# Performance work log

Measured on AMD Instinct MI355X. Metric: run time of the kernel, lower is better.

The kernel has to match this reference:

```python
import jax, jax.numpy as jnp
import numpy as np

B, T, H, W, C = 1, 16, 56, 56, 256
NH = 8
WS = (8, 7, 7)
SS = (4, 3, 3)
HID = 4 * C
N = WS[0] * WS[1] * WS[2]  # 392 tokens per window


def _rel_index(ws):
    wt, wh, ww = ws
    coords = np.stack(np.meshgrid(np.arange(wt), np.arange(wh), np.arange(ww), indexing='ij'))
    cf = coords.reshape(3, -1)
    rel = (cf[:, :, None] - cf[:, None, :]).transpose(1, 2, 0)
    rel[..., 0] += wt - 1
    rel[..., 1] += wh - 1
    rel[..., 2] += ww - 1
    rel[..., 0] *= (2 * wh - 1) * (2 * ww - 1)
    rel[..., 1] *= 2 * ww - 1
    return rel.sum(-1)  # (N, N) int


def _win_part_np(x, ws):
    b, t, h, w, c = x.shape
    x = x.reshape(b, t // ws[0], ws[0], h // ws[1], ws[1], w // ws[2], ws[2], c)
    return x.transpose(0, 1, 3, 5, 2, 4, 6, 7).reshape(-1, ws[0] * ws[1] * ws[2], c)


def _attn_mask(t, h, w, ws, ss):
    # static numpy construction of the shifted-window mask (nW, N, N)
    img = np.zeros((1, t, h, w, 1), dtype=np.float32)
    cnt = 0
    for d in (slice(-ws[0]), slice(-ws[0], -ss[0]), slice(-ss[0], None)):
        for hh in (slice(-ws[1]), slice(-ws[1], -ss[1]), slice(-ss[1], None)):
            for ww_ in (slice(-ws[2]), slice(-ws[2], -ss[2]), slice(-ss[2], None)):
                img[:, d, hh, ww_, :] = cnt
                cnt += 1
    mw = _win_part_np(img, ws).squeeze(-1)  # (nW, N)
    diff = mw[:, None, :] - mw[:, :, None]
    return np.where(diff != 0, np.float32(-100.0), np.float32(0.0))


_RPI = jnp.asarray(_rel_index(WS).reshape(-1))
_MASK = jnp.asarray(_attn_mask(T, H, W, WS, SS))  # (nW, N, N)


def _ln(x, g, b, eps=1e-5):
    mu = x.mean(-1, keepdims=True)
    var = ((x - mu) ** 2).mean(-1, keepdims=True)
    return (x - mu) * jax.lax.rsqrt(var + eps) * g + b


def _win_part(x, ws):
    b, t, h, w, c = x.shape
    x = x.reshape(b, t // ws[0], ws[0], h // ws[1], ws[1], w // ws[2], ws[2], c)
    return x.transpose(0, 1, 3, 5, 2, 4, 6, 7).reshape(-1, ws[0] * ws[1] * ws[2], c)


def _win_rev(win, ws, t, h, w):
    b = win.shape[0] // (t * h * w // (ws[0] * ws[1] * ws[2]))
    x = win.reshape(b, t // ws[0], h // ws[1], w // ws[2], ws[0], ws[1], ws[2], -1)
    return x.transpose(0, 1, 4, 2, 5, 3, 6, 7).reshape(b, t, h, w, -1)


def setup_inputs() -> dict:
    key = jax.random.key(0)
    ks = jax.random.split(key, 16)
    n_bias = (2 * WS[0] - 1) * (2 * WS[1] - 1) * (2 * WS[2] - 1)
    return {
        'x': jax.random.normal(ks[0], (B, T, H, W, C), jnp.float32),
        'norm1_g': jnp.ones((C,), jnp.float32),
        'norm1_b': jnp.zeros((C,), jnp.float32),
        'qkv_w': 0.02 * jax.random.normal(ks[1], (3 * C, C), jnp.float32),
        'qkv_b': jnp.zeros((3 * C,), jnp.float32),
        'rpb_table': 0.02 * jax.random.normal(ks[2], (n_bias, NH), jnp.float32),
        'proj_w': 0.02 * jax.random.normal(ks[3], (C, C), jnp.float32),
        'proj_b': jnp.zeros((C,), jnp.float32),
        'norm2_g': jnp.ones((C,), jnp.float32),
        'norm2_b': jnp.zeros((C,), jnp.float32),
        'fc1_w': 0.02 * jax.random.normal(ks[4], (HID, C), jnp.float32),
        'fc1_b': jnp.zeros((HID,), jnp.float32),
        'fc2_w': 0.02 * jax.random.normal(ks[5], (C, HID), jnp.float32),
        'fc2_b': jnp.zeros((C,), jnp.float32),
    }


def reference(x, norm1_g, norm1_b, qkv_w, qkv_b, rpb_table, proj_w, proj_b,
              norm2_g, norm2_b, fc1_w, fc1_b, fc2_w, fc2_b):
    hd = C // NH
    scale = hd ** -0.5
    shortcut = x
    h1 = _ln(x, norm1_g, norm1_b)
    # cyclic shift
    h1 = jnp.roll(h1, (-SS[0], -SS[1], -SS[2]), axis=(1, 2, 3))
    xw = _win_part(h1, WS)  # (B_, N, C)
    B_ = xw.shape[0]
    qkv = xw @ qkv_w.T + qkv_b  # (B_, N, 3C)
    qkv = qkv.reshape(B_, N, 3, NH, hd).transpose(2, 0, 3, 1, 4)
    q, k, v = qkv[0], qkv[1], qkv[2]  # (B_, NH, N, hd)
    attn = jnp.einsum('bhnd,bhmd->bhnm', q * scale, k)
    bias = rpb_table[_RPI].reshape(N, N, NH).transpose(2, 0, 1)  # (NH, N, N)
    attn = attn + bias[None]
    nW = _MASK.shape[0]
    attn = attn.reshape(B_ // nW, nW, NH, N, N) + _MASK[None, :, None]
    attn = jax.nn.softmax(attn, axis=-1).reshape(B_, NH, N, N)
    out = jnp.einsum('bhnm,bhmd->bhnd', attn, v).transpose(0, 2, 1, 3).reshape(B_, N, C)
    out = out @ proj_w.T + proj_b
    out = _win_rev(out, WS, T, H, W)
    out = jnp.roll(out, (SS[0], SS[1], SS[2]), axis=(1, 2, 3))
    x = shortcut + out
    # MLP with residual
    h2 = _ln(x, norm2_g, norm2_b)
    h2 = jax.nn.gelu(h2 @ fc1_w.T + fc1_b, approximate=False)
    return x + (h2 @ fc2_w.T + fc2_b)
```

## Files before the change

### kernel.cpp

```cpp
#include <hip/hip_runtime.h>
#include <hip/hip_bf16.h>
#include <cmath>

typedef unsigned short u16;
typedef unsigned int u32;

using bf16x8 = __attribute__((ext_vector_type(8))) short;
using f32x4  = __attribute__((ext_vector_type(4))) float;

__device__ __forceinline__ float b2f(u16 u) {
  union { u32 i; float f; } x; x.i = ((u32)u) << 16; return x.f;
}
__device__ __forceinline__ u16 f2b(float f) {
  union { float f; u32 i; } x; x.f = f;
  u32 r = x.i + 0x7fffu + ((x.i >> 16) & 1u);
  return (u16)(r >> 16);
}
__device__ __forceinline__ u32 cvtpk(float lo, float hi) {
  u32 r;
  asm("v_cvt_pk_bf16_f32 %0, %1, %2" : "=v"(r) : "v"(lo), "v"(hi));
  return r;
}
__device__ __forceinline__ float vexp2(float x) {
  float r;
  asm("v_exp_f32 %0, %1" : "=v"(r) : "v"(x));
  return r;
}
__device__ __forceinline__ void gload_lds16(const u16* g, u16* l) {
  __builtin_amdgcn_global_load_lds(
      (const __attribute__((address_space(1))) unsigned int*)g,
      (__attribute__((address_space(3))) unsigned int*)l, 16, 0, 0);
}

__global__ __launch_bounds__(256) void castw(const float* __restrict__ qkvw,
                                             const float* __restrict__ projw,
                                             const float* __restrict__ fc1w,
                                             const float* __restrict__ fc2w,
                                             u16* __restrict__ o) {
  int i = blockIdx.x * 256 + threadIdx.x;
  const float* src;
  int off;
  if (i < 196608)      { src = qkvw;  off = 0; }
  else if (i < 262144) { src = projw; off = 196608; }
  else if (i < 524288) { src = fc1w;  off = 262144; }
  else                 { src = fc2w;  off = 524288; }
  o[i] = f2b(src[i - off]);
}

__global__ __launch_bounds__(256) void bias_k(const float* __restrict__ rpb,
                                              u16* __restrict__ biasB,
                                              float* __restrict__ rowmax) {
  const int b = blockIdx.x;
  const int sl = b / 25, qt = b - sl * 25;
  const int head = sl & 7, cls = sl >> 3;
  const int tb = (cls >> 2) & 1, hb = (cls >> 1) & 1, wb = cls & 1;
  const int tid = threadIdx.x;
  const int lm = tid >> 4, kl = tid & 15;
  int q = qt * 16 + lm; if (q > 391) q = 391;
  const int ti = q / 49, rem = q - ti * 49, hi = rem / 7, wi = rem - hi * 7;
  const int cq = ti * 169 + hi * 13 + wi;
  const int rtq = tb ? (ti < 4 ? 1 : 2) : 0;
  const int rhq = hb ? (hi < 4 ? 1 : 2) : 0;
  const int rwq = wb ? (wi < 4 ? 1 : 2) : 0;
  const int labq = rtq * 9 + rhq * 3 + rwq;
  float mx = -3e38f;
  u16* ob = biasB + (size_t)b * 6400 + tid;
  for (int t = 0; t < 25; t++) {
    int k = t * 16 + kl;
    float v;
    if (k < 392) {
      int tk = k / 49, rk = k - tk * 49, hk = rk / 7, wk = rk - hk * 7;
      int ck = tk * 169 + hk * 13 + wk;
      float bv = rpb[(cq - ck + 1267) * 8 + head];
      int rt = tb ? (tk < 4 ? 1 : 2) : 0;
      int rh = hb ? (hk < 4 ? 1 : 2) : 0;
      int rw = wb ? (wk < 4 ? 1 : 2) : 0;
      if (rt * 9 + rh * 3 + rw != labq) bv -= 100.f;
      v = bv * 1.4426950408889634f;
      mx = fmaxf(mx, v);
    } else {
      v = -2081.f;
    }
    ob[t * 256] = f2b(v);
  }
  mx = fmaxf(mx, __shfl_xor(mx, 1, 64));
  mx = fmaxf(mx, __shfl_xor(mx, 2, 64));
  mx = fmaxf(mx, __shfl_xor(mx, 4, 64));
  mx = fmaxf(mx, __shfl_xor(mx, 8, 64));
  if (kl == 0) rowmax[sl * 392 + q] = mx;
}

__global__ __launch_bounds__(256) void ln_k(const float* __restrict__ src,
                                            const float* __restrict__ g,
                                            const float* __restrict__ b,
                                            u16* __restrict__ dst, int shifted) {
  const int wid = threadIdx.x >> 6, lane = threadIdx.x & 63;
  const int row = blockIdx.x * 4 + wid;
  int srow;
  if (shifted) {
    int widx = row / 392, n = row - widx * 392;
    int wt = widx >> 6, wh = (widx >> 3) & 7, ww = widx & 7;
    int ti = n / 49, rem = n - ti * 49, hi = rem / 7, wi = rem - hi * 7;
    int t = (wt * 8 + ti + 4) & 15;
    int h = wh * 7 + hi + 3; if (h >= 56) h -= 56;
    int w = ww * 7 + wi + 3; if (w >= 56) w -= 56;
    srow = (t * 56 + h) * 56 + w;
  } else {
    srow = row;
  }
  float4 v = *(const float4*)(src + (size_t)srow * 256 + lane * 4);
  float s = v.x + v.y + v.z + v.w;
  float sq = v.x * v.x + v.y * v.y + v.z * v.z + v.w * v.w;
  for (int o = 1; o < 64; o <<= 1) {
    s += __shfl_xor(s, o, 64);
    sq += __shfl_xor(sq, o, 64);
  }
  float mu = s * (1.0f / 256.0f);
  float rstd = rsqrtf(sq * (1.0f / 256.0f) - mu * mu + 1e-5f);
  float4 gg = *(const float4*)(g + lane * 4);
  float4 bb = *(const float4*)(b + lane * 4);
  ushort4 ov;
  ov.x = f2b((v.x - mu) * rstd * gg.x + bb.x);
  ov.y = f2b((v.y - mu) * rstd * gg.y + bb.y);
  ov.z = f2b((v.z - mu) * rstd * gg.z + bb.z);
  ov.w = f2b((v.w - mu) * rstd * gg.w + bb.w);
  *(ushort4*)(dst + (size_t)row * 256 + lane * 4) = ov;
}

template <int EPI>
__global__ __launch_bounds__(512) void gemm_k(const u16* __restrict__ A,
                                              const u16* __restrict__ Bw,
                                              int K, int tilesN,
                                              const float* __restrict__ bias,
                                              u16* __restrict__ outb,
                                              float* __restrict__ outf,
                                              const float* __restrict__ res,
                                              float qscale) {
  __shared__ __align__(16) u16 As[2][256 * 32];
  __shared__ __align__(16) u16 Bs[2][128 * 32];
  const int tid = threadIdx.x;
  const int swzb = ((int)blockIdx.x & 7) * ((int)gridDim.x >> 3) +
                   ((int)blockIdx.x >> 3);
  const int tm = swzb / tilesN, tn = swzb - tm * tilesN;
  const int wid = tid >> 6, lane = tid & 63;
  const int wm = wid >> 1, wn = wid & 1;
  const int lm = lane & 15, lk = lane >> 4;
  f32x4 acc[4][4] = {};
  const u16* Ap = A + (size_t)tm * 256 * K;
  const u16* Bp = Bw + (size_t)tn * 128 * K;

  const int sA0 = wid * 128;
  const int sB0 = wid * 64;
  const int nt = K >> 5;

#define STAGE(bufi, kk)                                                       \
  {                                                                           \
    int S = sA0 + lane, r = S >> 2, cs = S & 3;                               \
    gload_lds16(Ap + (size_t)r * K + (kk) + ((cs ^ ((r >> 1) & 3)) << 3),     \
                &As[bufi][sA0 * 8]);                                          \
    S = sA0 + 64 + lane; r = S >> 2; cs = S & 3;                              \
    gload_lds16(Ap + (size_t)r * K + (kk) + ((cs ^ ((r >> 1) & 3)) << 3),     \
                &As[bufi][(sA0 + 64) * 8]);                                   \
    S = sB0 + lane; r = S >> 2; cs = S & 3;                                   \
    gload_lds16(Bp + (size_t)r * K + (kk) + ((cs ^ ((r >> 1) & 3)) << 3),     \
                &Bs[bufi][sB0 * 8]);                                          \
  }

  STAGE(0, 0);
  __syncthreads();
  for (int t = 0; t < nt; t++) {
    const int cur = t & 1;
    if (t + 1 < nt) STAGE(cur ^ 1, (t + 1) << 5);
    bf16x8 af[4], bfr[4];
#pragma unroll
    for (int f = 0; f < 4; f++) {
      int ra = wm * 64 + f * 16 + lm;
      int rb = wn * 64 + f * 16 + lm;
      af[f] = *(const bf16x8*)((const char*)&As[cur][0] + ra * 64 +
                               ((lk ^ ((ra >> 1) & 3)) << 4));
      bfr[f] = *(const bf16x8*)((const char*)&Bs[cur][0] + rb * 64 +
                                ((lk ^ ((rb >> 1) & 3)) << 4));
    }
#pragma unroll
    for (int fm = 0; fm < 4; fm++)
#pragma unroll
      for (int fn = 0; fn < 4; fn++)
        acc[fm][fn] = __builtin_amdgcn_mfma_f32_16x16x32_bf16(
            af[fm], bfr[fn], acc[fm][fn], 0, 0, 0);
    __syncthreads();
  }
#undef STAGE

  const int rbase = tm * 256 + wm * 64, cbase = tn * 128 + wn * 64;
#pragma unroll
  for (int fm = 0; fm < 4; fm++) {
#pragma unroll
    for (int fn = 0; fn < 4; fn++) {
      const int col = cbase + fn * 16 + lm;
#pragma unroll
      for (int r = 0; r < 4; r++) {
        const int row = rbase + fm * 16 + lk * 4 + r;
        float v = acc[fm][fn][r] + bias[col];
        if (EPI == 0) {
          int s = col >> 8, rem = col & 255, head = rem >> 5, d = rem & 31;
          int widx = row / 392, n = row - widx * 392;
          size_t o;
          if (s == 2) {
            o = 25690112u + (((size_t)(widx * 8 + head)) * 32 + d) * 400 + n;
          } else {
            if (s == 0) v *= qscale;
            o = (size_t)s * 12845056u +
                (((size_t)(widx * 8 + head)) * 392 + n) * 32 + d;
          }
          outb[o] = f2b(v);
        } else if (EPI == 1) {
          int widx = row / 392, n = row - widx * 392;
          int wt = widx >> 6, wh = (widx >> 3) & 7, ww = widx & 7;
          int ti = n / 49, rem2 = n - ti * 49, hi = rem2 / 7, wi = rem2 - hi * 7;
          int t = (wt * 8 + ti + 4) & 15;
          int h = wh * 7 + hi + 3; if (h >= 56) h -= 56;
          int w = ww * 7 + wi + 3; if (w >= 56) w -= 56;
          size_t dr = ((size_t)(t * 56 + h)) * 56 + w;
          outf[dr * 256 + col] = res[dr * 256 + col] + v;
        } else if (EPI == 2) {
          float gv = 0.5f * v * (1.0f + erff(v * 0.70710678f));
          outb[(size_t)row * 1024 + col] = f2b(gv);
        } else {
          outf[(size_t)row * 256 + col] = res[(size_t)row * 256 + col] + v;
        }
      }
    }
  }
}

__global__ __launch_bounds__(256) void attn_k(const u16* __restrict__ qg,
                                              const u16* __restrict__ kg,
                                              const u16* __restrict__ vTg,
                                              const u16* __restrict__ biasB,
                                              const float* __restrict__ rowmax,
                                              u16* __restrict__ attno) {
  __shared__ __align__(16) char lds[60928];
  const int bid = blockIdx.x;
  const int widx = bid >> 3;
  const int tid = threadIdx.x;
  const size_t base = (size_t)bid * 12544;
  const int tb = (widx >> 6) & 1;
  const int hb = (((widx >> 3) & 7) == 7) ? 1 : 0;
  const int wb = ((widx & 7) == 7) ? 1 : 0;
  const int sl = (tb * 4 + hb * 2 + wb) * 8 + (bid & 7);
  const int VOFF = 25600;

#pragma unroll
  for (int i = 0; i < 6; i++) {
    int s = i * 256 + tid, r = s >> 2, cs = s & 3;
    gload_lds16(kg + base + r * 32 + ((cs ^ ((r >> 1) & 3)) << 3),
                (u16*)(lds + (size_t)(i * 256 + (tid & ~63)) * 16));
  }
  if (tid < 32) {
    int s = 1536 + tid, r = s >> 2, cs = s & 3;
    gload_lds16(kg + base + r * 32 + ((cs ^ ((r >> 1) & 3)) << 3),
                (u16*)(lds + (size_t)1536 * 16));
  }
  if (tid < 128) ((u32*)(lds + 25088))[tid] = 0u;
  {
    const u16* vsrc = vTg + (size_t)bid * 12800;
    for (int idx = tid; idx < 3200; idx += 256) {
      int d = idx / 100, c4 = idx - d * 100;
      *(ushort4*)(lds + VOFF + d * 848 + c4 * 8) =
          *(const ushort4*)(vsrc + d * 400 + c4 * 4);
    }
    for (int idx = tid; idx < 512; idx += 256) {
      int d = idx >> 4, e = idx & 15;
      *(u16*)(lds + VOFF + d * 848 + 800 + e * 2) = 0;
    }
  }
  __syncthreads();

  const int w = tid >> 6, lane = tid & 63;
  const int g = lane >> 4, lm = lane & 15;
  char* PqW = lds + 52736 + w * 2048 + lm * 128;
  const int swz = (lm & 7) << 4;
  const int kswz = ((lm >> 1) & 3);

  for (int qt = w; qt < 25; qt += 4) {
    const int q = qt * 16 + lm;
    const int qr = q < 391 ? q : 391;
    bf16x8 qf = *(const bf16x8*)(qg + base + (size_t)qr * 32 + g * 8);
    const u16* bp = biasB + ((size_t)(sl * 25 + qt) * 25) * 256 + lm * 16 + 4 * g;
    const float rmb = rowmax[sl * 392 + qr];
    f32x4 st[25];
#pragma unroll
    for (int t = 0; t < 25; t++) {
      ushort4 bb = *(const ushort4*)(bp + t * 256);
      f32x4 bacc = {b2f(bb.x), b2f(bb.y), b2f(bb.z), b2f(bb.w)};
      bf16x8 kf = *(const bf16x8*)(lds + (16 * t + lm) * 64 + ((g ^ kswz) << 4));
      st[t] = __builtin_amdgcn_mfma_f32_16x16x32_bf16(kf, qf, bacc, 0, 0, 0);
    }
    float m = -3e38f;
#pragma unroll
    for (int t = 0; t < 25; t++)
      m = fmaxf(m, fmaxf(fmaxf(st[t][0], st[t][1]), fmaxf(st[t][2], st[t][3])));
    m = fmaxf(m, __shfl_xor(m, 16, 64));
    m = fmaxf(m, __shfl_xor(m, 32, 64));
    m += rmb;

    float sum = 0.f;
    f32x4 oa0 = {0.f, 0.f, 0.f, 0.f}, oa1 = {0.f, 0.f, 0.f, 0.f};
#pragma unroll
    for (int p = 0; p < 6; p++) {
#pragma unroll
      for (int tl = 0; tl < 4; tl++) {
        int t = 4 * p + tl;
        float e0 = vexp2(st[t][0] - m), e1 = vexp2(st[t][1] - m);
        float e2 = vexp2(st[t][2] - m), e3 = vexp2(st[t][3] - m);
        sum += (e0 + e1) + (e2 + e3);
        uint2 pp;
        pp.x = cvtpk(e0, e1);
        pp.y = cvtpk(e2, e3);
        *(uint2*)(PqW + ((32 * tl + 8 * g) ^ swz)) = pp;
      }
      asm volatile("s_waitcnt lgkmcnt(0)" ::: "memory");
      __builtin_amdgcn_sched_barrier(0);
#pragma unroll
      for (int cl = 0; cl < 2; cl++) {
        int c = 2 * p + cl;
        bf16x8 pf = *(const bf16x8*)(PqW + ((64 * cl + 16 * g) ^ swz));
        const char* vrow = lds + VOFF + 64 * c + 16 * g;
        bf16x8 v0 = *(const bf16x8*)(vrow + lm * 848);
        bf16x8 v1 = *(const bf16x8*)(vrow + (16 + lm) * 848);
        oa0 = __builtin_amdgcn_mfma_f32_16x16x32_bf16(pf, v0, oa0, 0, 0, 0);
        oa1 = __builtin_amdgcn_mfma_f32_16x16x32_bf16(pf, v1, oa1, 0, 0, 0);
      }
      __builtin_amdgcn_sched_barrier(0);
    }
    {
      float e0 = vexp2(st[24][0] - m), e1 = vexp2(st[24][1] - m);
      float e2 = vexp2(st[24][2] - m), e3 = vexp2(st[24][3] - m);
      sum += (e0 + e1) + (e2 + e3);
      uint2 pp;
      pp.x = cvtpk(e0, e1);
      pp.y = cvtpk(e2, e3);
      *(uint2*)(PqW + ((8 * g) ^ swz)) = pp;
      uint2 zz; zz.x = 0u; zz.y = 0u;
      *(uint2*)(PqW + ((32 + 8 * g) ^ swz)) = zz;
      asm volatile("s_waitcnt lgkmcnt(0)" ::: "memory");
      __builtin_amdgcn_sched_barrier(0);
      bf16x8 pf = *(const bf16x8*)(PqW + ((16 * g) ^ swz));
      const char* vrow = lds + VOFF + 64 * 12 + 16 * g;
      bf16x8 v0 = *(const bf16x8*)(vrow + lm * 848);
      bf16x8 v1 = *(const bf16x8*)(vrow + (16 + lm) * 848);
      oa0 = __builtin_amdgcn_mfma_f32_16x16x32_bf16(pf, v0, oa0, 0, 0, 0);
      oa1 = __builtin_amdgcn_mfma_f32_16x16x32_bf16(pf, v1, oa1, 0, 0, 0);
      __builtin_amdgcn_sched_barrier(0);
    }
    sum += __shfl_xor(sum, 16, 64);
    sum += __shfl_xor(sum, 32, 64);
    const float inv = 1.f / sum;
#pragma unroll
    for (int r = 0; r < 4; r++) {
      int qq = qt * 16 + 4 * g + r;
      if (qq < 392) {
        u16* op = attno + ((size_t)(widx * 392 + qq)) * 256 + (bid & 7) * 32;
        op[lm] = f2b(oa0[r] * inv);
        op[16 + lm] = f2b(oa1[r] * inv);
      }
    }
  }
}

extern "C" void kernel_launch(void* const* d_in, const int* in_sizes, int n_in,
                              void* d_out, int out_size, void* d_ws,
                              size_t ws_size, hipStream_t stream) {
  const float* x     = (const float*)d_in[0];
  const float* n1g   = (const float*)d_in[1];
  const float* n1b   = (const float*)d_in[2];
  const float* qkvw  = (const float*)d_in[3];
  const float* qkvb  = (const float*)d_in[4];
  const float* rpb   = (const float*)d_in[5];
  const float* projw = (const float*)d_in[6];
  const float* projb = (const float*)d_in[7];
  const float* n2g   = (const float*)d_in[8];
  const float* n2b   = (const float*)d_in[9];
  const float* fc1w  = (const float*)d_in[10];
  const float* fc1b  = (const float*)d_in[11];
  const float* fc2w  = (const float*)d_in[12];
  const float* fc2b  = (const float*)d_in[13];

  const size_t NEED = 130547712;
  if (ws_size < NEED) return;

  char* ws = (char*)d_ws;
  u16* xw      = (u16*)(ws + 0LL);
  u16* qb      = (u16*)(ws + 25690112LL);
  u16* attno   = (u16*)(ws + 0LL);
  u16* hid     = (u16*)(ws + 0LL);
  u16* biasB   = (u16*)(ws + 103284736LL);
  float* rmx   = (float*)(ws + 123764736LL);
  u16* h2      = (u16*)(ws + 103284736LL);
  u16* wq      = (u16*)(ws + 128974848LL);
  u16* wp      = (u16*)(ws + 129368064LL);
  u16* w1      = (u16*)(ws + 129499136LL);
  u16* w2      = (u16*)(ws + 130023424LL);
  float* xres  = (float*)d_out;

  castw<<<3072, 256, 0, stream>>>(qkvw, projw, fc1w, fc2w, wq);
  bias_k<<<1600, 256, 0, stream>>>(rpb, biasB, rmx);

  ln_k<<<12544, 256, 0, stream>>>(x, n1g, n1b, xw, 1);
  gemm_k<0><<<196 * 6, 512, 0, stream>>>(
      xw, wq, 256, 6, qkvb, qb, nullptr, nullptr,
      0.17677669529663687f * 1.4426950408889634f);
  attn_k<<<1024, 256, 0, stream>>>(qb, qb + 12845056, qb + 2 * 12845056, biasB,
                                   rmx, attno);
  gemm_k<1><<<196 * 2, 512, 0, stream>>>(attno, wp, 256, 2, projb, nullptr,
                                         xres, x, 0.f);
  ln_k<<<12544, 256, 0, stream>>>(xres, n2g, n2b, h2, 0);
  gemm_k<2><<<196 * 8, 512, 0, stream>>>(h2, w1, 256, 8, fc1b, hid, nullptr,
                                         nullptr, 0.f);
  gemm_k<3><<<196 * 2, 512, 0, stream>>>(hid, w2, 1024, 2, fc2b, nullptr,
                                         (float*)d_out, xres, 0.f);
}
```

Before: 330.1 us.

## Redistribute softmax probabilities via ds_bpermute instead of LDS staging

```diff
diff --git a/kernel.cpp b/kernel.cpp
--- a/kernel.cpp
+++ b/kernel.cpp
@@ -25,6 +25,9 @@
   float r;
   asm("v_exp_f32 %0, %1" : "=v"(r) : "v"(x));
   return r;
+}
+__device__ __forceinline__ u32 bperm(int byteaddr, u32 v) {
+  return __builtin_amdgcn_ds_bpermute(byteaddr, v);
 }
 __device__ __forceinline__ void gload_lds16(const u16* g, u16* l) {
   __builtin_amdgcn_global_load_lds(
@@ -233,13 +236,11 @@
   }
 }
 
-__global__ __launch_bounds__(256) void attn_k(const u16* __restrict__ qg,
-                                              const u16* __restrict__ kg,
-                                              const u16* __restrict__ vTg,
-                                              const u16* __restrict__ biasB,
-                                              const float* __restrict__ rowmax,
-                                              u16* __restrict__ attno) {
-  __shared__ __align__(16) char lds[60928];
+__global__ __launch_bounds__(256, 3) void attn_k(
+    const u16* __restrict__ qg, const u16* __restrict__ kg,
+    const u16* __restrict__ vTg, const u16* __restrict__ biasB,
+    const float* __restrict__ rowmax, u16* __restrict__ attno) {
+  __shared__ __align__(16) char lds[52736];
   const int bid = blockIdx.x;
   const int widx = bid >> 3;
   const int tid = threadIdx.x;
@@ -278,9 +279,9 @@
 
   const int w = tid >> 6, lane = tid & 63;
   const int g = lane >> 4, lm = lane & 15;
-  char* PqW = lds + 52736 + w * 2048 + lm * 128;
-  const int swz = (lm & 7) << 4;
   const int kswz = ((lm >> 1) & 3);
+  const int srcA = (((lane >> 4) & 1) << 7) + (lm << 2);
+  const bool hi = (g >= 2);
 
   for (int qt = w; qt < 25; qt += 4) {
     const int q = qt * 16 + lm;
@@ -307,51 +308,35 @@
     float sum = 0.f;
     f32x4 oa0 = {0.f, 0.f, 0.f, 0.f}, oa1 = {0.f, 0.f, 0.f, 0.f};
 #pragma unroll
-    for (int p = 0; p < 6; p++) {
-#pragma unroll
-      for (int tl = 0; tl < 4; tl++) {
-        int t = 4 * p + tl;
-        float e0 = vexp2(st[t][0] - m), e1 = vexp2(st[t][1] - m);
-        float e2 = vexp2(st[t][2] - m), e3 = vexp2(st[t][3] - m);
-        sum += (e0 + e1) + (e2 + e3);
-        uint2 pp;
-        pp.x = cvtpk(e0, e1);
-        pp.y = cvtpk(e2, e3);
-        *(uint2*)(PqW + ((32 * tl + 8 * g) ^ swz)) = pp;
+    for (int c = 0; c < 13; c++) {
+      float e00 = vexp2(st[2 * c][0] - m), e01 = vexp2(st[2 * c][1] - m);
+      float e02 = vexp2(st[2 * c][2] - m), e03 = vexp2(st[2 * c][3] - m);
+      sum += (e00 + e01) + (e02 + e03);
+      u32 a0 = cvtpk(e00, e01), a1 = cvtpk(e02, e03);
+      u32 b0, b1;
+      if (c < 12) {
+        float e10 = vexp2(st[2 * c + 1][0] - m), e11 = vexp2(st[2 * c + 1][1] - m);
+        float e12 = vexp2(st[2 * c + 1][2] - m), e13 = vexp2(st[2 * c + 1][3] - m);
+        sum += (e10 + e11) + (e12 + e13);
+        b0 = cvtpk(e10, e11);
+        b1 = cvtpk(e12, e13);
+      } else {
+        b0 = 0u; b1 = 0u;
       }
-      asm volatile("s_waitcnt lgkmcnt(0)" ::: "memory");
-      __builtin_amdgcn_sched_barrier(0);
-#pragma unroll
-      for (int cl = 0; cl < 2; cl++) {
-        int c = 2 * p + cl;
-        bf16x8 pf = *(const bf16x8*)(PqW + ((64 * cl + 16 * g) ^ swz));
-        const char* vrow = lds + VOFF + 64 * c + 16 * g;
-        bf16x8 v0 = *(const bf16x8*)(vrow + lm * 848);
-        bf16x8 v1 = *(const bf16x8*)(vrow + (16 + lm) * 848);
-        oa0 = __builtin_amdgcn_mfma_f32_16x16x32_bf16(pf, v0, oa0, 0, 0, 0);
-        oa1 = __builtin_amdgcn_mfma_f32_16x16x32_bf16(pf, v1, oa1, 0, 0, 0);
-      }
-      __builtin_amdgcn_sched_barrier(0);
-    }
-    {
-      float e0 = vexp2(st[24][0] - m), e1 = vexp2(st[24][1] - m);
-      float e2 = vexp2(st[24][2] - m), e3 = vexp2(st[24][3] - m);
-      sum += (e0 + e1) + (e2 + e3);
-      uint2 pp;
-      pp.x = cvtpk(e0, e1);
-      pp.y = cvtpk(e2, e3);
-      *(uint2*)(PqW + ((8 * g) ^ swz)) = pp;
-      uint2 zz; zz.x = 0u; zz.y = 0u;
-      *(uint2*)(PqW + ((32 + 8 * g) ^ swz)) = zz;
-      asm volatile("s_waitcnt lgkmcnt(0)" ::: "memory");
-      __builtin_amdgcn_sched_barrier(0);
-      bf16x8 pf = *(const bf16x8*)(PqW + ((16 * g) ^ swz));
-      const char* vrow = lds + VOFF + 64 * 12 + 16 * g;
+      u32 A0 = bperm(srcA, a0), B0 = bperm(srcA, b0);
+      u32 A1 = bperm(srcA, a1), B1 = bperm(srcA, b1);
+      u32 A2 = bperm(srcA + 64, a0), B2 = bperm(srcA + 64, b0);
+      u32 A3 = bperm(srcA + 64, a1), B3 = bperm(srcA + 64, b1);
+      union { u32 u[4]; bf16x8 v; } P;
+      P.u[0] = hi ? B0 : A0;
+      P.u[1] = hi ? B1 : A1;
+      P.u[2] = hi ? B2 : A2;
+      P.u[3] = hi ? B3 : A3;
+      const char* vrow = lds + VOFF + 64 * c + 16 * g;
       bf16x8 v0 = *(const bf16x8*)(vrow + lm * 848);
       bf16x8 v1 = *(const bf16x8*)(vrow + (16 + lm) * 848);
-      oa0 = __builtin_amdgcn_mfma_f32_16x16x32_bf16(pf, v0, oa0, 0, 0, 0);
-      oa1 = __builtin_amdgcn_mfma_f32_16x16x32_bf16(pf, v1, oa1, 0, 0, 0);
-      __builtin_amdgcn_sched_barrier(0);
+      oa0 = __builtin_amdgcn_mfma_f32_16x16x32_bf16(P.v, v0, oa0, 0, 0, 0);
+      oa1 = __builtin_amdgcn_mfma_f32_16x16x32_bf16(P.v, v1, oa1, 0, 0, 0);
     }
     sum += __shfl_xor(sum, 16, 64);
     sum += __shfl_xor(sum, 32, 64);
```

Result: slower. 471.5 us (+42.9%).

## Fuse LayerNorm2, FC1+GELU and FC2 into a single MLP kernel

Applied to the files above, without the earlier changes.

```diff
diff --git a/kernel.cpp b/kernel.cpp
--- a/kernel.cpp
+++ b/kernel.cpp
@@ -213,7 +213,7 @@
                 (((size_t)(widx * 8 + head)) * 392 + n) * 32 + d;
           }
           outb[o] = f2b(v);
-        } else if (EPI == 1) {
+        } else {
           int widx = row / 392, n = row - widx * 392;
           int wt = widx >> 6, wh = (widx >> 3) & 7, ww = widx & 7;
           int ti = n / 49, rem2 = n - ti * 49, hi = rem2 / 7, wi = rem2 - hi * 7;
@@ -222,12 +222,149 @@
           int w = ww * 7 + wi + 3; if (w >= 56) w -= 56;
           size_t dr = ((size_t)(t * 56 + h)) * 56 + w;
           outf[dr * 256 + col] = res[dr * 256 + col] + v;
-        } else if (EPI == 2) {
+        }
+      }
+    }
+  }
+}
+
+__global__ __launch_bounds__(256) void mlp_k(const float* __restrict__ xres,
+                                             const u16* __restrict__ w1,
+                                             const float* __restrict__ b1,
+                                             const u16* __restrict__ w2,
+                                             const float* __restrict__ b2,
+                                             const float* __restrict__ n2g,
+                                             const float* __restrict__ n2b,
+                                             float* __restrict__ out) {
+  __shared__ __align__(16) char lds[65536];
+  char* Abuf = lds;
+  char* Hs = lds + 32768;
+  u16* Ws = (u16*)(lds + 49152);
+
+  const int tid = threadIdx.x;
+  const int swzb = ((int)blockIdx.x & 7) * ((int)gridDim.x >> 3) +
+                   ((int)blockIdx.x >> 3);
+  const int row0 = swzb * 64;
+  const int w = tid >> 6, lane = tid & 63;
+  const int lm = lane & 15, g = lane >> 4;
+
+  {
+    float4 gg = *(const float4*)(n2g + lane * 4);
+    float4 bb = *(const float4*)(n2b + lane * 4);
+    for (int rr = 0; rr < 16; rr++) {
+      int r = w * 16 + rr;
+      float4 v = *(const float4*)(xres + (size_t)(row0 + r) * 256 + lane * 4);
+      float s = v.x + v.y + v.z + v.w;
+      float sq = v.x * v.x + v.y * v.y + v.z * v.z + v.w * v.w;
+      for (int o = 1; o < 64; o <<= 1) {
+        s += __shfl_xor(s, o, 64);
+        sq += __shfl_xor(sq, o, 64);
+      }
+      float mu = s * (1.0f / 256.0f);
+      float rstd = rsqrtf(sq * (1.0f / 256.0f) - mu * mu + 1e-5f);
+      uint2 pp;
+      pp.x = cvtpk((v.x - mu) * rstd * gg.x + bb.x,
+                   (v.y - mu) * rstd * gg.y + bb.y);
+      pp.y = cvtpk((v.z - mu) * rstd * gg.z + bb.z,
+                   (v.w - mu) * rstd * gg.w + bb.w);
+      *(uint2*)(Abuf + r * 512 + (((lane >> 1) ^ (r & 7)) << 4) +
+                ((lane & 1) << 3)) = pp;
+    }
+  }
+
+  f32x4 acc2[4][4] = {};
+  for (int j = 0; j < 8; j++) {
+    f32x4 acc1[4][2] = {};
+    for (int ks = 0; ks < 8; ks++) {
+      __syncthreads();
+      {
+        int i0 = w * 64 + lane;
+#pragma unroll
+        for (int it = 0; it < 2; it++) {
+          int idx = it * 256 + i0, r = idx >> 2, s = idx & 3;
+          gload_lds16(w1 + (size_t)(j * 128 + r) * 256 + ks * 32 +
+                          ((s ^ (r & 3)) << 3),
+                      Ws + (size_t)(it * 256 + w * 64) * 8);
+        }
+      }
+      __syncthreads();
+      bf16x8 af[4], bfr[2];
+#pragma unroll
+      for (int f = 0; f < 4; f++) {
+        int ra = f * 16 + lm;
+        af[f] = *(const bf16x8*)(Abuf + ra * 512 +
+                                 (((ks * 4 + g) ^ (ra & 7)) << 4));
+      }
+#pragma unroll
+      for (int f = 0; f < 2; f++) {
+        int rb = w * 32 + f * 16 + lm;
+        bfr[f] = *(const bf16x8*)((const char*)Ws + rb * 64 +
+                                  ((g ^ (rb & 3)) << 4));
+      }
+#pragma unroll
+      for (int fm = 0; fm < 4; fm++)
+#pragma unroll
+        for (int fn = 0; fn < 2; fn++)
+          acc1[fm][fn] = __builtin_amdgcn_mfma_f32_16x16x32_bf16(
+              af[fm], bfr[fn], acc1[fm][fn], 0, 0, 0);
+    }
+#pragma unroll
+    for (int fn = 0; fn < 2; fn++) {
+      int col = w * 32 + fn * 16 + lm;
+      float bv = b1[j * 128 + col];
+#pragma unroll
+      for (int fm = 0; fm < 4; fm++) {
+#pragma unroll
+        for (int r = 0; r < 4; r++) {
+          float v = acc1[fm][fn][r] + bv;
           float gv = 0.5f * v * (1.0f + erff(v * 0.70710678f));
-          outb[(size_t)row * 1024 + col] = f2b(gv);
-        } else {
-          outf[(size_t)row * 256 + col] = res[(size_t)row * 256 + col] + v;
+          int row = fm * 16 + g * 4 + r;
+          *(u16*)(Hs + row * 256 + ((((col >> 3) ^ (row & 7))) << 4) +
+                  ((col & 7) << 1)) = f2b(gv);
         }
+      }
+    }
+    for (int ks = 0; ks < 4; ks++) {
+      __syncthreads();
+      {
+        int i0 = w * 64 + lane;
+#pragma unroll
+        for (int it = 0; it < 4; it++) {
+          int idx = it * 256 + i0, r = idx >> 2, s = idx & 3;
+          gload_lds16(w2 + (size_t)r * 1024 + j * 128 + ks * 32 +
+                          ((s ^ (r & 3)) << 3),
+                      Ws + (size_t)(it * 256 + w * 64) * 8);
+        }
+      }
+      __syncthreads();
+      bf16x8 af[4], bfr[4];
+#pragma unroll
+      for (int f = 0; f < 4; f++) {
+        int ra = f * 16 + lm;
+        af[f] = *(const bf16x8*)(Hs + ra * 256 +
+                                 (((ks * 4 + g) ^ (ra & 7)) << 4));
+        int rb = w * 64 + f * 16 + lm;
+        bfr[f] = *(const bf16x8*)((const char*)Ws + rb * 64 +
+                                  ((g ^ (rb & 3)) << 4));
+      }
+#pragma unroll
+      for (int fm = 0; fm < 4; fm++)
+#pragma unroll
+        for (int fn = 0; fn < 4; fn++)
+          acc2[fm][fn] = __builtin_amdgcn_mfma_f32_16x16x32_bf16(
+              af[fm], bfr[fn], acc2[fm][fn], 0, 0, 0);
+    }
+  }
+#pragma unroll
+  for (int fm = 0; fm < 4; fm++) {
+#pragma unroll
+    for (int fn = 0; fn < 4; fn++) {
+      int col = w * 64 + fn * 16 + lm;
+      float bv = b2[col];
+#pragma unroll
+      for (int r = 0; r < 4; r++) {
+        size_t o = (size_t)(row0 + fm * 16 + g * 4 + r) * 256 + col;
+        out[o] = xres[o] + acc2[fm][fn][r] + bv;
       }
     }
   }
@@ -393,10 +530,8 @@
   u16* xw      = (u16*)(ws + 0LL);
   u16* qb      = (u16*)(ws + 25690112LL);
   u16* attno   = (u16*)(ws + 0LL);
-  u16* hid     = (u16*)(ws + 0LL);
   u16* biasB   = (u16*)(ws + 103284736LL);
   float* rmx   = (float*)(ws + 123764736LL);
-  u16* h2      = (u16*)(ws + 103284736LL);
   u16* wq      = (u16*)(ws + 128974848LL);
   u16* wp      = (u16*)(ws + 129368064LL);
   u16* w1      = (u16*)(ws + 129499136LL);
@@ -414,9 +549,6 @@
                                    rmx, attno);
   gemm_k<1><<<196 * 2, 512, 0, stream>>>(attno, wp, 256, 2, projb, nullptr,
                                          xres, x, 0.f);
-  ln_k<<<12544, 256, 0, stream>>>(xres, n2g, n2b, h2, 0);
-  gemm_k<2><<<196 * 8, 512, 0, stream>>>(h2, w1, 256, 8, fc1b, hid, nullptr,
-                                         nullptr, 0.f);
-  gemm_k<3><<<196 * 2, 512, 0, stream>>>(hid, w2, 1024, 2, fc2b, nullptr,
-                                         (float*)d_out, xres, 0.f);
-}
+  mlp_k<<<784, 256, 0, stream>>>(xres, w1, fc1b, w2, fc2b, n2g, n2b,
+                                 (float*)d_out);
+}
```

After: 362.6 us. +9.9%, slower.
